# Kernel tuning notes

Measured on AMD Instinct MI355X. Metric: run time of the kernel, lower is better.

## Reference

```python
import jax, jax.numpy as jnp
import numpy as np

B, T, D, H = 8, 1024, 512, 8
QD, PD, POSD, VD, K = 32, 4, 48, 64, 31
FF = 4 * D
FF1, FF2, FF3, NLA = FF * 3 // 4, FF, FF * 5 // 4, D * 3 // 4


def _swoosh_l(x):
    return jax.nn.softplus(x - 4.0) - 0.08 * x - 0.035


def _swoosh_r(x):
    return jax.nn.softplus(x - 1.0) - 0.08 * x - 0.313261687


def setup_inputs() -> dict:
    key = jax.random.key(0)
    ks = iter(jax.random.split(key, 64))

    def w(shape, fan_in):
        return jax.random.normal(next(ks), shape, jnp.float32) * (fan_in ** -0.5)

    inp = {
        'x': jax.random.normal(next(ks), (B, T, D), jnp.float32),
        'pos_emb': jax.random.normal(next(ks), (2 * T - 1, POSD), jnp.float32),
        'mask': jnp.ones((B, T), bool),
        'attw_q_w': w((D, H * QD), D), 'attw_k_w': w((D, H * QD), D),
        'attw_pq_w': w((D, H * PD), D), 'attw_pos_w': w((POSD, H * PD), POSD),
        'ff1_in_w': w((D, FF1), D), 'ff1_in_b': jnp.zeros(FF1),
        'ff1_out_w': w((FF1, D), FF1), 'ff1_out_b': jnp.zeros(D),
        'nla_w': w((D, NLA * 3), D), 'nla_b': jnp.zeros(NLA * 3),
        'nla_out_w': w((NLA, D), NLA), 'nla_out_b': jnp.zeros(D),
        'sa1_v_w': w((D, H * VD), D), 'sa1_v_b': jnp.zeros(H * VD),
        'sa1_o_w': w((H * VD, D), H * VD), 'sa1_o_b': jnp.zeros(D),
        'conv1_in_w': w((D, 2 * D), D), 'conv1_in_b': jnp.zeros(2 * D),
        'conv1_dw_w': w((D, 1, K), K), 'conv1_dw_b': jnp.zeros(D),
        'conv1_out_w': w((D, D), D), 'conv1_out_b': jnp.zeros(D),
        'ff2_in_w': w((D, FF2), D), 'ff2_in_b': jnp.zeros(FF2),
        'ff2_out_w': w((FF2, D), FF2), 'ff2_out_b': jnp.zeros(D),
        'mid_scale': jax.random.uniform(next(ks), (D,), jnp.float32),
        'sa2_v_w': w((D, H * VD), D), 'sa2_v_b': jnp.zeros(H * VD),
        'sa2_o_w': w((H * VD, D), H * VD), 'sa2_o_b': jnp.zeros(D),
        'conv2_in_w': w((D, 2 * D), D), 'conv2_in_b': jnp.zeros(2 * D),
        'conv2_dw_w': w((D, 1, K), K), 'conv2_dw_b': jnp.zeros(D),
        'conv2_out_w': w((D, D), D), 'conv2_out_b': jnp.zeros(D),
        'ff3_in_w': w((D, FF3), D), 'ff3_in_b': jnp.zeros(FF3),
        'ff3_out_w': w((FF3, D), FF3), 'ff3_out_b': jnp.zeros(D),
        'norm_bias': jnp.zeros(D), 'norm_log_scale': jnp.zeros(()),
        'out_scale': jax.random.uniform(next(ks), (D,), jnp.float32),
    }
    return inp


def _forward(x, pos_emb, attw_q_w, attw_k_w, attw_pq_w, attw_pos_w,
             ff1_in_w, ff1_in_b, ff1_out_w, ff1_out_b,
             nla_w, nla_b, nla_out_w, nla_out_b,
             sa1_v_w, sa1_v_b, sa1_o_w, sa1_o_b,
             conv1_in_w, conv1_in_b, conv1_dw_w, conv1_dw_b, conv1_out_w, conv1_out_b,
             ff2_in_w, ff2_in_b, ff2_out_w, ff2_out_b,
             mid_scale,
             sa2_v_w, sa2_v_b, sa2_o_w, sa2_o_b,
             conv2_in_w, conv2_in_b, conv2_dw_w, conv2_dw_b, conv2_out_w, conv2_out_b,
             ff3_in_w, ff3_in_b, ff3_out_w, ff3_out_b,
             norm_bias, norm_log_scale, out_scale, mask):
    res = x
    # --- relative-pos multi-head attention weights ---
    q = (x @ attw_q_w).reshape(B, T, H, QD).transpose(0, 2, 1, 3)
    k = (x @ attw_k_w).reshape(B, T, H, QD).transpose(0, 2, 1, 3)
    p = (x @ attw_pq_w).reshape(B, T, H, PD).transpose(0, 2, 1, 3)
    content = jnp.einsum('bhtd,bhsd->bhts', q, k) * (QD ** -0.5)
    rel = (pos_emb @ attw_pos_w).reshape(2 * T - 1, H, PD).transpose(1, 0, 2)
    idx = jnp.arange(T)[:, None] - jnp.arange(T)[None, :] + (T - 1)
    relg = rel[:, idx]  # [H, T, T, PD]
    scores = content + jnp.einsum('bhtd,htsd->bhts', p, relg)
    scores = jnp.where(mask[:, None, None, :], scores, -10000.0)
    attn = jax.nn.softmax(scores, axis=-1)
    attn = jnp.where(mask[:, None, :, None], attn, 0.0)

    def mk(y):
        return jnp.where(mask[..., None], y, 0.0)

    def ff(y, wi, bi, wo, bo):
        return _swoosh_l(y @ wi + bi) @ wo + bo

    def sa(y, vw, vb, ow, ob):
        v = (y @ vw + vb).reshape(B, T, H, VD).transpose(0, 2, 1, 3)
        o = jnp.einsum('bhts,bhsd->bhtd', attn, v).transpose(0, 2, 1, 3).reshape(B, T, H * VD)
        return o @ ow + ob

    def conv(y, iw, ib, dw, db, ow, ob):
        u = y @ iw + ib
        a, g = jnp.split(u, 2, axis=-1)
        a = (a * jax.nn.sigmoid(g)).transpose(0, 2, 1)  # [B, D, T]
        a = jnp.where(mask[:, None, :], a, 0.0)
        c = jax.lax.conv_general_dilated(a, dw, (1,), [(K // 2, K // 2)],
                                         dimension_numbers=('NCH', 'OIH', 'NCH'),
                                         feature_group_count=D) + db[None, :, None]
        c = _swoosh_r(c.transpose(0, 2, 1))
        return mk(c @ ow + ob)

    def bypass(r, u, s):
        s = jnp.clip(s, 0.2, 1.0)  # eval/steady regime
        return r + (u - r) * s

    x = mk(x + ff(x, ff1_in_w, ff1_in_b, ff1_out_w, ff1_out_b))
    # non-linear attention (uses head 0)
    a, b, c = jnp.split(x @ nla_w + nla_b, 3, axis=-1)
    att0 = jnp.einsum('bts,bsd->btd', attn[:, 0], jnp.tanh(b) * c)
    x = mk(x + ((a * att0) @ nla_out_w + nla_out_b))
    x = mk(x + sa(x, sa1_v_w, sa1_v_b, sa1_o_w, sa1_o_b))
    x = mk(x + conv(x, conv1_in_w, conv1_in_b, conv1_dw_w, conv1_dw_b, conv1_out_w, conv1_out_b))
    x = mk(x + ff(x, ff2_in_w, ff2_in_b, ff2_out_w, ff2_out_b))
    x = mk(bypass(res, x, mid_scale))
    x = mk(x + sa(x, sa2_v_w, sa2_v_b, sa2_o_w, sa2_o_b))
    x = mk(x + conv(x, conv2_in_w, conv2_in_b, conv2_dw_w, conv2_dw_b, conv2_out_w, conv2_out_b))
    x = mk(x + ff(x, ff3_in_w, ff3_in_b, ff3_out_w, ff3_out_b))
    # BiasNorm
    rms = jnp.sqrt(jnp.mean((x - norm_bias) ** 2, axis=-1, keepdims=True) + 1e-8)
    x = x / rms * jnp.exp(norm_log_scale)
    x = mk(bypass(res, x, out_scale))
    return x


def reference(x, pos_emb, mask, attw_q_w, attw_k_w, attw_pq_w, attw_pos_w,
              ff1_in_w, ff1_in_b, ff1_out_w, ff1_out_b,
              nla_w, nla_b, nla_out_w, nla_out_b,
              sa1_v_w, sa1_v_b, sa1_o_w, sa1_o_b,
              conv1_in_w, conv1_in_b, conv1_dw_w, conv1_dw_b, conv1_out_w, conv1_out_b,
              ff2_in_w, ff2_in_b, ff2_out_w, ff2_out_b,
              mid_scale,
              sa2_v_w, sa2_v_b, sa2_o_w, sa2_o_b,
              conv2_in_w, conv2_in_b, conv2_dw_w, conv2_dw_b, conv2_out_w, conv2_out_b,
              ff3_in_w, ff3_in_b, ff3_out_w, ff3_out_b,
              norm_bias, norm_log_scale, out_scale):
    return _forward(x, pos_emb, attw_q_w, attw_k_w, attw_pq_w, attw_pos_w,
                    ff1_in_w, ff1_in_b, ff1_out_w, ff1_out_b,
                    nla_w, nla_b, nla_out_w, nla_out_b,
                    sa1_v_w, sa1_v_b, sa1_o_w, sa1_o_b,
                    conv1_in_w, conv1_in_b, conv1_dw_w, conv1_dw_b, conv1_out_w, conv1_out_b,
                    ff2_in_w, ff2_in_b, ff2_out_w, ff2_out_b,
                    mid_scale,
                    sa2_v_w, sa2_v_b, sa2_o_w, sa2_o_b,
                    conv2_in_w, conv2_in_b, conv2_dw_w, conv2_dw_b, conv2_out_w, conv2_out_b,
                    ff3_in_w, ff3_in_b, ff3_out_w, ff3_out_b,
                    norm_bias, norm_log_scale, out_scale, mask)
```

## Files before the change

### kernel.cpp

```cpp
#include <hip/hip_runtime.h>
#include <hip/hip_bf16.h>
#include <math.h>

using bf16 = __hip_bfloat16;
using f16 = _Float16;
typedef short s16x8 __attribute__((ext_vector_type(8)));
typedef f16   f16x2 __attribute__((ext_vector_type(2)));
typedef float f32x4 __attribute__((ext_vector_type(4)));
typedef unsigned int u32;
#define DEV __device__ __forceinline__
#define AS1 __attribute__((address_space(1)))
#define AS3 __attribute__((address_space(3)))

constexpr int Bc = 8, Tc = 1024, Dc = 512, Hc = 8;
constexpr int QDc = 32, PDc = 4, POSDc = 48, VDc = 64;
constexpr int Nrow = Bc * Tc;
constexpr int KWc = 31;
constexpr float LOG2E = 1.4426950408889634f;

DEV float frcp(float x) { return __builtin_amdgcn_rcpf(x); }
DEV float softplus_f(float y) { return fmaxf(y, 0.f) + __logf(1.f + __expf(-fabsf(y))); }
DEV float swoosh_l_f(float x) { return softplus_f(x - 4.f) - 0.08f * x - 0.035f; }
DEV float swoosh_r_f(float x) { return softplus_f(x - 1.f) - 0.08f * x - 0.313261687f; }
DEV float sigmoid_f(float x)  { return frcp(1.f + __expf(-x)); }
DEV float tanh_f(float x) {
  float e = __expf(2.f * fminf(fmaxf(x, -15.f), 15.f));
  return (e - 1.f) * frcp(e + 1.f);
}
DEV float clip_s(float s)     { return fminf(fmaxf(s, 0.2f), 1.0f); }
DEV float to_f(bf16 x)  { return __bfloat162float(x); }
DEV float b2f(short s) { union { u32 u; float f; } z; z.u = (u32)(unsigned short)s << 16; return z.f; }
DEV short f2bb(float v) { bf16 h = __float2bfloat16(v); return *(short*)&h; }
DEV unsigned short f2h(float v) { f16 h = (f16)v; union { f16 x; unsigned short s; } z; z.x = h; return z.s; }
DEV float h2f(unsigned short s) { union { unsigned short s; f16 x; } z; z.s = s; return (float)z.x; }
DEV u32 packbf(float a, float b) {
  return ((u32)(unsigned short)f2bb(b) << 16) | (u32)(unsigned short)f2bb(a);
}
DEV float dot2(u32 a, u32 b, float c) {
#if __has_builtin(__builtin_amdgcn_fdot2)
  union { u32 u; f16x2 v; } x, y; x.u = a; y.u = b;
  return __builtin_amdgcn_fdot2(x.v, y.v, c, false);
#else
  return c + h2f(a & 0xffff) * h2f(b & 0xffff) + h2f(a >> 16) * h2f(b >> 16);
#endif
}

DEV float wave_sum(float v) {
#pragma unroll
  for (int o = 32; o > 0; o >>= 1) v += __shfl_xor(v, o);
  return v;
}

DEV void gload16(const void* g, void* l) {
  __builtin_amdgcn_global_load_lds((const AS1 u32*)g, (AS3 u32*)l, 16, 0, 0);
}

template <int ACT, int WM, int WN, int FM, int FN>
__global__ __launch_bounds__(256) void gemm_mfma(
    const bf16* __restrict__ A, const bf16* __restrict__ B,
    const float* __restrict__ bias, const float* __restrict__ resid,
    float* __restrict__ Cf, bf16* __restrict__ Cb, bf16* __restrict__ Cb2,
    const bf16* __restrict__ auxb, const float* __restrict__ auxf,
    const float* __restrict__ auxf2,
    int M, int N, int K, int lda, int ldb, int ldc,
    long sAz, long sBo, long sBi, long sCo, long sCi, int nh) {
  constexpr int BM = WM * FM * 16, BN = WN * FN * 16;
  constexpr int NPA = (ACT == 8) ? 3 : 1;
  constexpr int NPB = (ACT == 2) ? 2 : 1;
  constexpr int PANA = 384, PANB = 512;
  constexpr int ASZT = NPA * BM * 128;
  constexpr int BUF = (NPA * BM + NPB * BN) * 128;
  constexpr int LPS = NPA * (BM / 32) + NPB * (BN / 32);

  int z = blockIdx.z;
  int zo = z / nh, zi = z - zo * nh;
  A += (long)z * sAz;
  B += (long)zo * sBo + (long)zi * sBi;
  long coff = (long)zo * sCo + (long)zi * sCi;

  __shared__ char lds[2 * BUF];

  int tid = threadIdx.x;
  int lane = tid & 63, w = tid >> 6;
  int wm = w / WN, wn = w % WN;

  int gx = gridDim.x;
  int nwg = gx * gridDim.y;
  int flat = blockIdx.y * gx + blockIdx.x;
  if ((nwg & 7) == 0) flat = (flat & 7) * (nwg >> 3) + (flat >> 3);
  int m0 = (flat / gx) * BM, n0 = (flat % gx) * BN;

  int lrow = lane >> 3, lch = lane & 7;
  const bf16* ga = A + (long)(m0 + w * (BM / 4) + lrow) * lda + ((lch ^ lrow) << 3);
  const bf16* gb = B + (long)(n0 + w * (BN / 4) + lrow) * ldb + ((lch ^ lrow) << 3);

  f32x4 acc[NPA * NPB][FM][FN];
#pragma unroll
  for (int p = 0; p < NPA * NPB; ++p)
#pragma unroll
    for (int i = 0; i < FM; ++i)
#pragma unroll
      for (int j = 0; j < FN; ++j) acc[p][i][j] = 0.f;

  int nt = K >> 6;
  {
#pragma unroll
    for (int pa = 0; pa < NPA; ++pa) {
      const bf16* gp = ga + (long)(pa * PANA) * lda;
      char* la = lds + pa * BM * 128 + w * (BM / 4) * 128;
#pragma unroll
      for (int i = 0; i < BM / 32; ++i) gload16(gp + (long)(i * 8) * lda, la + i * 1024);
    }
#pragma unroll
    for (int pb = 0; pb < NPB; ++pb) {
      const bf16* gp = gb + (long)(pb * PANB) * ldb;
      char* lb = lds + ASZT + pb * BN * 128 + w * (BN / 4) * 128;
#pragma unroll
      for (int i = 0; i < BN / 32; ++i) gload16(gp + (long)(i * 8) * ldb, lb + i * 1024);
    }
  }

  for (int t = 0; t < nt; ++t) {
    char* cA = lds + (t & 1) * BUF;
    if (t + 1 < nt) {
      int k0 = (t + 1) << 6;
      char* base = lds + ((t + 1) & 1) * BUF;
#pragma unroll
      for (int pa = 0; pa < NPA; ++pa) {
        const bf16* gp = ga + (long)(pa * PANA) * lda + k0;
        char* la = base + pa * BM * 128 + w * (BM / 4) * 128;
#pragma unroll
        for (int i = 0; i < BM / 32; ++i) gload16(gp + (long)(i * 8) * lda, la + i * 1024);
      }
#pragma unroll
      for (int pb = 0; pb < NPB; ++pb) {
        const bf16* gp = gb + (long)(pb * PANB) * ldb + k0;
        char* lb = base + ASZT + pb * BN * 128 + w * (BN / 4) * 128;
#pragma unroll
        for (int i = 0; i < BN / 32; ++i) gload16(gp + (long)(i * 8) * ldb, lb + i * 1024);
      }
      asm volatile("s_waitcnt vmcnt(%0)" :: "n"(LPS) : "memory");
    } else {
      asm volatile("s_waitcnt vmcnt(0)" ::: "memory");
    }
    __builtin_amdgcn_s_barrier();
    __builtin_amdgcn_sched_barrier(0);
#pragma unroll
    for (int ks = 0; ks < 2; ++ks) {
      int cg = ks * 4 + (lane >> 4);
      s16x8 af[NPA][FM], bfr[NPB][FN];
#pragma unroll
      for (int pa = 0; pa < NPA; ++pa)
#pragma unroll
        for (int f = 0; f < FM; ++f) {
          int row = wm * FM * 16 + f * 16 + (lane & 15);
          af[pa][f] = *(const s16x8*)(cA + pa * BM * 128 + row * 128 +
                                      ((cg ^ (row & 7)) << 4));
        }
#pragma unroll
      for (int pb = 0; pb < NPB; ++pb)
#pragma unroll
        for (int f = 0; f < FN; ++f) {
          int row = wn * FN * 16 + f * 16 + (lane & 15);
          bfr[pb][f] = *(const s16x8*)(cA + ASZT + pb * BN * 128 + row * 128 +
                                       ((cg ^ (row & 7)) << 4));
        }
#pragma unroll
      for (int pa = 0; pa < NPA; ++pa)
#pragma unroll
        for (int pb = 0; pb < NPB; ++pb)
#pragma unroll
          for (int fm = 0; fm < FM; ++fm)
#pragma unroll
            for (int fn = 0; fn < FN; ++fn)
              acc[pa * NPB + pb][fm][fn] = __builtin_amdgcn_mfma_f32_16x16x32_bf16(
                  af[pa][fm], bfr[pb][fn], acc[pa * NPB + pb][fm][fn], 0, 0, 0);
    }
    __builtin_amdgcn_sched_barrier(0);
    __builtin_amdgcn_s_barrier();
  }

  int rbase = m0 + wm * FM * 16 + (lane >> 4) * 4;
  int cbase = n0 + wn * FN * 16 + (lane & 15);
#pragma unroll
  for (int fn = 0; fn < FN; ++fn) {
    int col = cbase + fn * 16;
    if (col >= N) continue;
#pragma unroll
    for (int fm = 0; fm < FM; ++fm) {
#pragma unroll
      for (int r = 0; r < 4; ++r) {
        int row = rbase + fm * 16 + r;
        if (row >= M) continue;
        long ci = coff + (long)row * ldc + col;
        if constexpr (ACT == 2) {
          float va = acc[0][fm][fn][r] + bias[col];
          float vg = acc[1][fm][fn][r] + bias[col + 512];
          Cb[ci] = __float2bfloat16(va * sigmoid_f(vg));
        } else if constexpr (ACT == 4) {
          float a = to_f(auxb[(long)col * 8192 + (long)zo * 1024 + row]);
          Cb[ci] = __float2bfloat16(acc[0][fm][fn][r] * a);
        } else if constexpr (ACT == 5) {
          float v = acc[0][fm][fn][r] + bias[col] + resid[ci];
          float rv = auxf[ci];
          float o = rv + (v - rv) * clip_s(auxf2[col]);
          Cf[ci] = o;
          Cb[ci] = __float2bfloat16(o);
        } else if constexpr (ACT == 7) {
          Cb[ci] = __float2bfloat16(acc[0][fm][fn][r] + bias[row]);
        } else if constexpr (ACT == 8) {
          float va = acc[0][fm][fn][r] + bias[row];
          float vb = acc[1][fm][fn][r] + bias[row + 384];
          float vc = acc[2][fm][fn][r] + bias[row + 768];
          Cb2[ci] = __float2bfloat16(va);
          Cb[ci] = __float2bfloat16(tanh_f(vb) * vc);
        } else if constexpr (ACT == 9) {
          float v = acc[0][fm][fn][r];
          if (col < 512) {
            Cb2[(long)row * 512 + col] = __float2bfloat16(v);
          } else {
            Cb[(long)row * ldc + (col - 512)] =
                __float2bfloat16(swoosh_l_f(v + bias[col - 512]));
          }
        } else {
          float v = acc[0][fm][fn][r] + (bias ? bias[col] : 0.f);
          if (ACT == 1) v = swoosh_l_f(v);
          if (resid) v += resid[ci];
          if (Cf) Cf[ci] = v;
          if (Cb) Cb[ci] = __float2bfloat16(v);
        }
      }
    }
  }
}

__global__ __launch_bounds__(256) void relph_kernel(
    const float* __restrict__ pos_emb, const float* __restrict__ Wpos,
    float* __restrict__ relb,
    const float* __restrict__ x0, const float* __restrict__ Wpq,
    f16* __restrict__ ph) {
  int zz = blockIdx.z;
  const float* A  = zz ? x0 : pos_emb;
  const float* Bm = zz ? Wpq : Wpos;
  int M = zz ? Nrow : (2 * Tc - 1);
  int K = zz ? Dc : POSDc;
  int lda = K;
  int m0 = blockIdx.y * 64;
  if (m0 >= M) return;

  __shared__ float As[16][72];
  __shared__ float Bs[16][72];
  int tid = threadIdx.x;
  int tx = tid & 15, ty = tid >> 4;
  int arow = tid >> 2, ak4 = (tid & 3) * 4;
  int bk = tid >> 4, bn4 = (tid & 15) * 4;
  float acc[4][4] = {};
  for (int k0 = 0; k0 < K; k0 += 16) {
    int gm = m0 + arow;
#pragma unroll
    for (int j = 0; j < 4; ++j) {
      int gk = k0 + ak4 + j;
      As[ak4 + j][arow] = (gm < M && gk < K) ? A[(long)gm * lda + gk] : 0.f;
    }
    int gk = k0 + bk;
#pragma unroll
    for (int j = 0; j < 4; ++j) {
      int gn = bn4 + j;
      Bs[bk][bn4 + j] = (gk < K && gn < 32) ? Bm[(long)gk * 32 + gn] : 0.f;
    }
    __syncthreads();
#pragma unroll
    for (int kk = 0; kk < 16; ++kk) {
      float a4[4], b4[4];
#pragma unroll
      for (int i = 0; i < 4; ++i) a4[i] = As[kk][ty * 4 + i];
#pragma unroll
      for (int i = 0; i < 4; ++i) b4[i] = Bs[kk][tx * 4 + i];
#pragma unroll
      for (int i = 0; i < 4; ++i)
#pragma unroll
        for (int j = 0; j < 4; ++j) acc[i][j] += a4[i] * b4[j];
    }
    __syncthreads();
  }
#pragma unroll
  for (int i = 0; i < 4; ++i) {
    int gm = m0 + ty * 4 + i;
    if (gm >= M) continue;
#pragma unroll
    for (int j = 0; j < 4; ++j) {
      int gn = tx * 4 + j;
      if (gn < 32) {
        if (zz) ph[(long)gm * 32 + gn] = (f16)(acc[i][j] * LOG2E);
        else    relb[(long)gm * 32 + gn] = acc[i][j];
      }
    }
  }
}

struct TDesc { const float* src; bf16* dst; int K, N, tile0, ntx; float scale; };
struct TBatch { TDesc d[18]; int n; };

__global__ __launch_bounds__(256) void transpose_batch_kernel(TBatch tb) {
  int tile = blockIdx.x;
  int wi = 0;
#pragma unroll 1
  for (int i = 1; i < 18; ++i)
    if (i < tb.n && tb.d[i].tile0 <= tile) wi = i;
  const float* W = tb.d[wi].src;
  bf16* WT = tb.d[wi].dst;
  int K = tb.d[wi].K, N = tb.d[wi].N;
  float sc = tb.d[wi].scale;
  int lt = tile - tb.d[wi].tile0;
  int ntx = tb.d[wi].ntx;
  int bx = (lt % ntx) * 32, by = (lt / ntx) * 32;

  __shared__ float t[32][33];
  int lx = threadIdx.x & 31, ly = threadIdx.x >> 5;
#pragma unroll
  for (int j = 0; j < 4; ++j) {
    int k = by + ly + j * 8, n = bx + lx;
    if (k < K && n < N) t[ly + j * 8][lx] = W[(long)k * N + n];
  }
  __syncthreads();
#pragma unroll
  for (int j = 0; j < 4; ++j) {
    int n = bx + ly + j * 8, k = by + lx;
    if (n < N && k < K) WT[(long)n * K + k] = __float2bfloat16(t[lx][ly + j * 8] * sc);
  }
}

__global__ void dw_transpose_kernel(const float* __restrict__ dw1, float* __restrict__ o1,
                                    const float* __restrict__ dw2, float* __restrict__ o2) {
  int i = blockIdx.x * 256 + threadIdx.x;
  if (i >= 2 * 512 * KWc) return;
  const float* s = (i < 512 * KWc) ? dw1 : dw2;
  float* o = (i < 512 * KWc) ? o1 : o2;
  int j = (i < 512 * KWc) ? i : i - 512 * KWc;
  int d = j / KWc, kk = j - d * KWc;
  o[kk * 512 + d] = s[j];
}

__global__ void f2b_kernel(const float* __restrict__ in, bf16* __restrict__ out, int nOct) {
  int i = blockIdx.x * 256 + threadIdx.x;
  if (i >= nOct) return;
  float4 a = *(const float4*)(in + (long)i * 8);
  float4 b = *(const float4*)(in + (long)i * 8 + 4);
  s16x8 o;
  o[0] = f2bb(a.x); o[1] = f2bb(a.y); o[2] = f2bb(a.z); o[3] = f2bb(a.w);
  o[4] = f2bb(b.x); o[5] = f2bb(b.y); o[6] = f2bb(b.z); o[7] = f2bb(b.w);
  *(s16x8*)((short*)out + (long)i * 8) = o;
}

__global__ __launch_bounds__(256) void scores_softmax_fused(
    const bf16* __restrict__ qk, const f16* __restrict__ ph,
    const float* __restrict__ rel, bf16* __restrict__ attn) {
  int bh = blockIdx.y;
  int h = bh & (Hc - 1), b = bh >> 3;
  int t0 = blockIdx.x * 16;
  int tid = threadIdx.x, lane = tid & 63, w = tid >> 6;

  __shared__ unsigned short eS[16 * 1024];
  __shared__ u32 rel01[1040], rel23[1040];
  __shared__ u32 pS[16][2];
  __shared__ float lS[16][4];

  for (int i = tid; i < 1039; i += 256) {
    float4 rv = *(const float4*)(rel + (long)(t0 + i) * 32 + h * 4);
    rel01[i] = ((u32)f2h(rv.y) << 16) | f2h(rv.x);
    rel23[i] = ((u32)f2h(rv.w) << 16) | f2h(rv.z);
  }
  if (tid < 16) {
    const u32* pp = (const u32*)(ph + ((long)(b * Tc + t0 + tid)) * 32 + h * 4);
    pS[tid][0] = pp[0]; pS[tid][1] = pp[1];
  }
  __syncthreads();

  s16x8 af = *(const s16x8*)(qk + ((long)(b * Tc + t0 + (lane & 15))) * 512 +
                             h * QDc + (lane >> 4) * 8);
  int g = lane >> 4;
  u32 p01[4], p23[4];
#pragma unroll
  for (int r = 0; r < 4; ++r) { p01[r] = pS[g * 4 + r][0]; p23[r] = pS[g * 4 + r][1]; }
  float sum[4] = {0.f, 0.f, 0.f, 0.f};
  f32x4 zero = {0.f, 0.f, 0.f, 0.f};
  int cols0 = w * 256;
#pragma unroll 4
  for (int tile = 0; tile < 16; ++tile) {
    int s0 = cols0 + tile * 16;
    s16x8 bfr = *(const s16x8*)(qk + ((long)(b * Tc + s0 + (lane & 15))) * 512 +
                                256 + h * QDc + (lane >> 4) * 8);
    f32x4 acc = __builtin_amdgcn_mfma_f32_16x16x32_bf16(af, bfr, zero, 0, 0, 0);
    int scol = s0 + (lane & 15);
    int idx0 = g * 4 - scol + 1023;
#pragma unroll
    for (int r = 0; r < 4; ++r) {
      int idx = idx0 + r;
      float pos = dot2(p23[r], rel23[idx], dot2(p01[r], rel01[idx], 0.f));
      float e = exp2f(acc[r] + pos);
      sum[r] += e;
      *(unsigned short*)((char*)eS + (g * 4 + r) * 2048 + ((scol * 2) ^ (g << 5))) =
          (unsigned short)f2bb(e);
    }
  }
#pragma unroll
  for (int o = 1; o < 16; o <<= 1)
#pragma unroll
    for (int r = 0; r < 4; ++r) sum[r] += __shfl_xor(sum[r], o);
  if ((lane & 15) == 0) {
#pragma unroll
    for (int r = 0; r < 4; ++r) lS[g * 4 + r][w] = sum[r];
  }
  __syncthreads();

#pragma unroll
  for (int rr = 0; rr < 4; ++rr) {
    int row = w * 4 + rr;
    float inv = frcp(lS[row][0] + lS[row][1] + lS[row][2] + lS[row][3]);
    int mask = ((row >> 2) & 3) << 5;
    char* rowbase = (char*)eS + row * 2048;
    u32* grow = (u32*)(attn + ((long)bh * Tc + t0 + row) * Tc);
#pragma unroll
    for (int k = 0; k < 8; ++k) {
      u32 ew = *(u32*)(rowbase + (((lane + k * 64) * 4) ^ mask));
      grow[lane + k * 64] = packbf(b2f((short)(ew & 0xffff)) * inv,
                                   b2f((short)(ew >> 16)) * inv);
    }
  }
}

__global__ __launch_bounds__(256) void dwconv_kernel(
    const bf16* __restrict__ a, const float* __restrict__ dwT,
    const float* __restrict__ db, bf16* __restrict__ c) {
  int i = blockIdx.x * 256 + threadIdx.x;
  int oct = i & 63, bt = i >> 6;
  int t = bt & (Tc - 1), b0 = bt - t;
  float acc0 = db[oct * 8 + 0], acc1 = db[oct * 8 + 1], acc2 = db[oct * 8 + 2],
        acc3 = db[oct * 8 + 3], acc4 = db[oct * 8 + 4], acc5 = db[oct * 8 + 5],
        acc6 = db[oct * 8 + 6], acc7 = db[oct * 8 + 7];
#pragma unroll
  for (int kk = 0; kk < KWc; ++kk) {
    int tt = t + kk - (KWc / 2);
    if ((unsigned)tt < (unsigned)Tc) {
      s16x8 av = *(const s16x8*)((const short*)a + ((long)(b0 + tt) << 9) + oct * 8);
      const float* wp = dwT + kk * 512 + oct * 8;
      float4 w0 = *(const float4*)wp, w1 = *(const float4*)(wp + 4);
      acc0 += b2f(av[0]) * w0.x; acc1 += b2f(av[1]) * w0.y;
      acc2 += b2f(av[2]) * w0.z; acc3 += b2f(av[3]) * w0.w;
      acc4 += b2f(av[4]) * w1.x; acc5 += b2f(av[5]) * w1.y;
      acc6 += b2f(av[6]) * w1.z; acc7 += b2f(av[7]) * w1.w;
    }
  }
  s16x8 o;
  o[0] = f2bb(swoosh_r_f(acc0)); o[1] = f2bb(swoosh_r_f(acc1));
  o[2] = f2bb(swoosh_r_f(acc2)); o[3] = f2bb(swoosh_r_f(acc3));
  o[4] = f2bb(swoosh_r_f(acc4)); o[5] = f2bb(swoosh_r_f(acc5));
  o[6] = f2bb(swoosh_r_f(acc6)); o[7] = f2bb(swoosh_r_f(acc7));
  *(s16x8*)((short*)c + (long)bt * 512 + oct * 8) = o;
}

__global__ __launch_bounds__(256) void rmsnorm_bypass_kernel(
    const float* __restrict__ x, const float* __restrict__ x0,
    const float* __restrict__ nb, const float* __restrict__ nls,
    const float* __restrict__ os, float* __restrict__ out) {
  int row = blockIdx.x;
  int tid = threadIdx.x;
  const float* xr = x + (long)row * 512;
  const float* rr = x0 + (long)row * 512;
  float* orow = out + (long)row * 512;
  float v0 = xr[tid], v1 = xr[tid + 256];
  float d0 = v0 - nb[tid], d1 = v1 - nb[tid + 256];
  float ss = d0 * d0 + d1 * d1;
  __shared__ float red[4];
  int lane = tid & 63, wid = tid >> 6;
  ss = wave_sum(ss);
  if (lane == 0) red[wid] = ss;
  __syncthreads();
  ss = red[0] + red[1] + red[2] + red[3];
  float rms = sqrtf(ss * (1.f / 512.f) + 1e-8f);
  float scl = expf(nls[0]) / rms;
  float r0 = rr[tid], s0 = clip_s(os[tid]);
  orow[tid] = r0 + (v0 * scl - r0) * s0;
  float r1 = rr[tid + 256], s1 = clip_s(os[tid + 256]);
  orow[tid + 256] = r1 + (v1 * scl - r1) * s1;
}

static inline int cdiv(int a, int b) { return (a + b - 1) / b; }

template <int ACT, int WM = 2, int WN = 2, int FM = 2, int FN = 2>
static void mfma_launch(hipStream_t st, const bf16* A, const bf16* B, const float* bias,
                        const float* resid, float* Cf, bf16* Cb, bf16* Cb2,
                        const bf16* auxb, const float* auxf, const float* auxf2,
                        int M, int N, int K, int lda, int ldb, int ldc,
                        int Z = 1, int nh = 1, long sAz = 0, long sBo = 0, long sBi = 0,
                        long sCo = 0, long sCi = 0) {
  dim3 grid(cdiv(N, WN * FN * 16), cdiv(M, WM * FM * 16), Z);
  gemm_mfma<ACT, WM, WN, FM, FN><<<grid, dim3(256), 0, st>>>(
      A, B, bias, resid, Cf, Cb, Cb2, auxb, auxf, auxf2, M, N, K, lda, ldb, ldc,
      sAz, sBo, sBi, sCo, sCi, nh);
}
#define MFMA_AV 2, 2, 2, 2

extern "C" void kernel_launch(void* const* d_in, const int* in_sizes, int n_in,
                              void* d_out, int out_size, void* d_ws, size_t ws_size,
                              hipStream_t stream) {
  const float* x0        = (const float*)d_in[0];
  const float* pos_emb   = (const float*)d_in[1];
  const float* Wq        = (const float*)d_in[3];
  const float* Wk        = (const float*)d_in[4];
  const float* Wpq       = (const float*)d_in[5];
  const float* Wpos      = (const float*)d_in[6];
  const float* ff1_in_w  = (const float*)d_in[7];
  const float* ff1_in_b  = (const float*)d_in[8];
  const float* ff1_out_w = (const float*)d_in[9];
  const float* ff1_out_b = (const float*)d_in[10];
  const float* nla_w     = (const float*)d_in[11];
  const float* nla_b     = (const float*)d_in[12];
  const float* nla_out_w = (const float*)d_in[13];
  const float* nla_out_b = (const float*)d_in[14];
  const float* sa1_v_w   = (const float*)d_in[15];
  const float* sa1_v_b   = (const float*)d_in[16];
  const float* sa1_o_w   = (const float*)d_in[17];
  const float* sa1_o_b   = (const float*)d_in[18];
  const float* cv1_in_w  = (const float*)d_in[19];
  const float* cv1_in_b  = (const float*)d_in[20];
  const float* cv1_dw_w  = (const float*)d_in[21];
  const float* cv1_dw_b  = (const float*)d_in[22];
  const float* cv1_out_w = (const float*)d_in[23];
  const float* cv1_out_b = (const float*)d_in[24];
  const float* ff2_in_w  = (const float*)d_in[25];
  const float* ff2_in_b  = (const float*)d_in[26];
  const float* ff2_out_w = (const float*)d_in[27];
  const float* ff2_out_b = (const float*)d_in[28];
  const float* mid_scale = (const float*)d_in[29];
  const float* sa2_v_w   = (const float*)d_in[30];
  const float* sa2_v_b   = (const float*)d_in[31];
  const float* sa2_o_w   = (const float*)d_in[32];
  const float* sa2_o_b   = (const float*)d_in[33];
  const float* cv2_in_w  = (const float*)d_in[34];
  const float* cv2_in_b  = (const float*)d_in[35];
  const float* cv2_dw_w  = (const float*)d_in[36];
  const float* cv2_dw_b  = (const float*)d_in[37];
  const float* cv2_out_w = (const float*)d_in[38];
  const float* cv2_out_b = (const float*)d_in[39];
  const float* ff3_in_w  = (const float*)d_in[40];
  const float* ff3_in_b  = (const float*)d_in[41];
  const float* ff3_out_w = (const float*)d_in[42];
  const float* ff3_out_b = (const float*)d_in[43];
  const float* norm_bias = (const float*)d_in[44];
  const float* nls       = (const float*)d_in[45];
  const float* out_scale = (const float*)d_in[46];
  float* out = (float*)d_out;

  char* wsb = (char*)d_ws;
  size_t off = 0;
  bf16* attn  = (bf16*)(wsb + off); off += (size_t)Bc * Hc * Tc * Tc * 2;
  float* xA   = (float*)(wsb + off); off += (size_t)Nrow * Dc * 4;
  float* xB   = (float*)(wsb + off); off += (size_t)Nrow * Dc * 4;
  bf16*  xb   = (bf16*)(wsb + off);  off += (size_t)Nrow * Dc * 2;
  bf16*  x0b  = (bf16*)(wsb + off);  off += (size_t)Nrow * Dc * 2;
  bf16*  big1b = (bf16*)(wsb + off); off += (size_t)Nrow * 2560 * 2;
  bf16*  big2b = (bf16*)(wsb + off); off += (size_t)Nrow * Dc * 2;
  bf16*  wT    = (bf16*)(wsb + off); off += (size_t)9961472 * 2;
  float* dwT1  = (float*)(wsb + off); off += (size_t)KWc * 512 * 4;
  float* dwT2  = (float*)(wsb + off); off += (size_t)KWc * 512 * 4;
  bf16*  tbcT  = (bf16*)(wsb + off); off += (size_t)384 * Nrow * 2;
  bf16* big3b = big1b + (size_t)Nrow * 2048;
  bf16* vT    = big2b;
  bf16* qkb   = big2b;
  bf16* aT    = big1b;
  f16*  ph    = (f16*)(big1b + (size_t)Nrow * 1536);
  float* relb = (float*)(ph + (size_t)Nrow * 32);

  bf16* p_w = wT;
  auto alloc_w = [&](int n, int k) { bf16* r = p_w; p_w += (size_t)n * k; return r; };
  bf16* qkff1_wT   = alloc_w(2048, 512);
  bf16* ff1_out_wT = alloc_w(512, 1536);
  bf16* nla_wT     = alloc_w(1152, 512);
  bf16* nla_out_wT = alloc_w(512, 384);
  bf16* sa1_v_wT   = alloc_w(512, 512);
  bf16* sa1_o_wT   = alloc_w(512, 512);
  bf16* cv1_in_wT  = alloc_w(1024, 512);
  bf16* cv1_out_wT = alloc_w(512, 512);
  bf16* ff2_in_wT  = alloc_w(2048, 512);
  bf16* ff2_out_wT = alloc_w(512, 2048);
  bf16* sa2_v_wT   = alloc_w(512, 512);
  bf16* sa2_o_wT   = alloc_w(512, 512);
  bf16* cv2_in_wT  = alloc_w(1024, 512);
  bf16* cv2_out_wT = alloc_w(512, 512);
  bf16* ff3_in_wT  = alloc_w(2560, 512);
  bf16* ff3_out_wT = alloc_w(512, 2560);

  const int nOctD = Nrow * 64;

  f2b_kernel<<<cdiv(nOctD, 256), 256, 0, stream>>>(x0, x0b, nOctD);
  {
    TBatch tb{};
    auto add = [&](int idx, const float* s, bf16* d, int K, int N, int& t0, float sc) {
      tb.d[idx] = {s, d, K, N, t0, cdiv(N, 32), sc};
      t0 += cdiv(N, 32) * cdiv(K, 32);
    };
    int t0 = 0;
    add(0,  Wq,        qkff1_wT,   512, 256,  t0, 0.17677669529663687f * LOG2E);
    add(1,  Wk,        qkff1_wT + (size_t)256 * 512, 512, 256, t0, 1.f);
    add(2,  ff1_in_w,  qkff1_wT + (size_t)512 * 512, 512, 1536, t0, 1.f);
    add(3,  ff1_out_w, ff1_out_wT, 1536, 512, t0, 1.f);
    add(4,  nla_w,     nla_wT,     512, 1152, t0, 1.f);
    add(5,  nla_out_w, nla_out_wT, 384, 512,  t0, 1.f);
    add(6,  sa1_v_w,   sa1_v_wT,   512, 512,  t0, 1.f);
    add(7,  sa1_o_w,   sa1_o_wT,   512, 512,  t0, 1.f);
    add(8,  cv1_in_w,  cv1_in_wT,  512, 1024, t0, 1.f);
    add(9,  cv1_out_w, cv1_out_wT, 512, 512,  t0, 1.f);
    add(10, ff2_in_w,  ff2_in_wT,  512, 2048, t0, 1.f);
    add(11, ff2_out_w, ff2_out_wT, 2048, 512, t0, 1.f);
    add(12, sa2_v_w,   sa2_v_wT,   512, 512,  t0, 1.f);
    add(13, sa2_o_w,   sa2_o_wT,   512, 512,  t0, 1.f);
    add(14, cv2_in_w,  cv2_in_wT,  512, 1024, t0, 1.f);
    add(15, cv2_out_w, cv2_out_wT, 512, 512,  t0, 1.f);
    add(16, ff3_in_w,  ff3_in_wT,  512, 2560, t0, 1.f);
    add(17, ff3_out_w, ff3_out_wT, 2560, 512, t0, 1.f);
    tb.n = 18;
    transpose_batch_kernel<<<t0, 256, 0, stream>>>(tb);
  }
  dw_transpose_kernel<<<cdiv(2 * 512 * KWc, 256), 256, 0, stream>>>(
      cv1_dw_w, dwT1, cv2_dw_w, dwT2);
  relph_kernel<<<dim3(1, 128, 2), 256, 0, stream>>>(pos_emb, Wpos, relb, x0, Wpq, ph);

  mfma_launch<9>(stream, x0b, qkff1_wT, ff1_in_b, nullptr, nullptr, big1b, qkb,
                 nullptr, nullptr, nullptr, Nrow, 2048, 512, 512, 512, 1536);
  scores_softmax_fused<<<dim3(Tc / 16, 64), 256, 0, stream>>>(qkb, ph, relb, attn);

  mfma_launch<0>(stream, big1b, ff1_out_wT, ff1_out_b, x0, xA, xb, nullptr,
                 nullptr, nullptr, nullptr, Nrow, 512, 1536, 1536, 1536, 512);

  mfma_launch<8>(stream, nla_wT, xb, nla_b, nullptr, nullptr, tbcT, aT,
                 nullptr, nullptr, nullptr, 384, Nrow, 512, 512, 512, Nrow);
  mfma_launch<4>(stream, attn, tbcT, nullptr, nullptr, nullptr, big3b, nullptr,
                 aT, nullptr, nullptr, Tc, 384, Tc, Tc, Nrow, 384,
                 Bc, 1, (long)Hc * Tc * Tc, 1024, 0, (long)Tc * 384, 0);
  mfma_launch<0>(stream, big3b, nla_out_wT, nla_out_b, xA, xB, xb, nullptr,
                 nullptr, nullptr, nullptr, Nrow, 512, 384, 384, 384, 512);

  mfma_launch<7>(stream, sa1_v_wT, xb, sa1_v_b, nullptr, nullptr, vT, nullptr,
                 nullptr, nullptr, nullptr, 512, Nrow, 512, 512, 512, Nrow);
  mfma_launch<0, MFMA_AV>(stream, attn, vT, nullptr, nullptr, nullptr, big3b, nullptr,
                          nullptr, nullptr, nullptr, Tc, VDc, Tc, Tc, Nrow, 512,
                          Bc * Hc, Hc, (long)Tc * Tc, Tc, (long)VDc * Nrow,
                          (long)Tc * 512, VDc);
  mfma_launch<0>(stream, big3b, sa1_o_wT, sa1_o_b, xB, xA, xb, nullptr,
                 nullptr, nullptr, nullptr, Nrow, 512, 512, 512, 512, 512);

  mfma_launch<2>(stream, xb, cv1_in_wT, cv1_in_b, nullptr, nullptr, big2b, nullptr,
                 nullptr, nullptr, nullptr, Nrow, 512, 512, 512, 512, 512);
  dwconv_kernel<<<cdiv(nOctD, 256), 256, 0, stream>>>(big2b, dwT1, cv1_dw_b, big3b);
  mfma_launch<0>(stream, big3b, cv1_out_wT, cv1_out_b, xA, xB, xb, nullptr,
                 nullptr, nullptr, nullptr, Nrow, 512, 512, 512, 512, 512);

  mfma_launch<1>(stream, xb, ff2_in_wT, ff2_in_b, nullptr, nullptr, big1b, nullptr,
                 nullptr, nullptr, nullptr, Nrow, 2048, 512, 512, 512, 2048);
  mfma_launch<5>(stream, big1b, ff2_out_wT, ff2_out_b, xB, xB, xb, nullptr,
                 nullptr, x0, mid_scale, Nrow, 512, 2048, 2048, 2048, 512);

  mfma_launch<7>(stream, sa2_v_wT, xb, sa2_v_b, nullptr, nullptr, vT, nullptr,
                 nullptr, nullptr, nullptr, 512, Nrow, 512, 512, 512, Nrow);
  mfma_launch<0, MFMA_AV>(stream, attn, vT, nullptr, nullptr, nullptr, big3b, nullptr,
                          nullptr, nullptr, nullptr, Tc, VDc, Tc, Tc, Nrow, 512,
                          Bc * Hc, Hc, (long)Tc * Tc, Tc, (long)VDc * Nrow,
                          (long)Tc * 512, VDc);
  mfma_launch<0>(stream, big3b, sa2_o_wT, sa2_o_b, xB, xA, xb, nullptr,
                 nullptr, nullptr, nullptr, Nrow, 512, 512, 512, 512, 512);

  mfma_launch<2>(stream, xb, cv2_in_wT, cv2_in_b, nullptr, nullptr, big2b, nullptr,
                 nullptr, nullptr, nullptr, Nrow, 512, 512, 512, 512, 512);
  dwconv_kernel<<<cdiv(nOctD, 256), 256, 0, stream>>>(big2b, dwT2, cv2_dw_b, big3b);
  mfma_launch<0>(stream, big3b, cv2_out_wT, cv2_out_b, xA, xB, xb, nullptr,
                 nullptr, nullptr, nullptr, Nrow, 512, 512, 512, 512, 512);

  mfma_launch<1>(stream, xb, ff3_in_wT, ff3_in_b, nullptr, nullptr, big1b, nullptr,
                 nullptr, nullptr, nullptr, Nrow, 2560, 512, 512, 512, 2560);
  mfma_launch<0>(stream, big1b, ff3_out_wT, ff3_out_b, xB, xA, nullptr, nullptr,
                 nullptr, nullptr, nullptr, Nrow, 512, 2560, 2560, 2560, 512);

  rmsnorm_bypass_kernel<<<Nrow, 256, 0, stream>>>(xA, x0, norm_bias, nls, out_scale, out);
}
```

Before: 765.7 us.

## Defer softmax normalization to consumer GEMM epilogues and precompute fp16 relative-position table

The scores kernel now writes unnormalized exp values and stores per-row inverse sums in a small buffer. The three downstream GEMMs that consume the attention matrix (NLA and both value products) apply the 1/l scale in their epilogues. The relative-position bias is also packed to fp16 pairs per head by relph_kernel, so the scores kernel reads it from global memory instead of staging it through shared memory. This removes per-element multiplies and the LDS staging loop in the softmax kernel, at the cost of extra global loads in the epilogues and uncached per-element relative-position reads.

```diff
diff --git a/kernel.cpp b/kernel.cpp
--- a/kernel.cpp
+++ b/kernel.cpp
@@ -199,7 +199,7 @@
           Cb[ci] = __float2bfloat16(va * sigmoid_f(vg));
         } else if constexpr (ACT == 4) {
           float a = to_f(auxb[(long)col * 8192 + (long)zo * 1024 + row]);
-          Cb[ci] = __float2bfloat16(acc[0][fm][fn][r] * a);
+          Cb[ci] = __float2bfloat16(acc[0][fm][fn][r] * a * auxf[(long)zo * 8192 + row]);
         } else if constexpr (ACT == 5) {
           float v = acc[0][fm][fn][r] + bias[col] + resid[ci];
           float rv = auxf[ci];
@@ -222,6 +222,8 @@
             Cb[(long)row * ldc + (col - 512)] =
                 __float2bfloat16(swoosh_l_f(v + bias[col - 512]));
           }
+        } else if constexpr (ACT == 10) {
+          Cb[ci] = __float2bfloat16(acc[0][fm][fn][r] * auxf[(long)z * 1024 + row]);
         } else {
           float v = acc[0][fm][fn][r] + (bias ? bias[col] : 0.f);
           if (ACT == 1) v = swoosh_l_f(v);
@@ -236,7 +238,7 @@
 
 __global__ __launch_bounds__(256) void relph_kernel(
     const float* __restrict__ pos_emb, const float* __restrict__ Wpos,
-    float* __restrict__ relb,
+    uint2* __restrict__ relh,
     const float* __restrict__ x0, const float* __restrict__ Wpq,
     f16* __restrict__ ph) {
   int zz = blockIdx.z;
@@ -283,17 +285,26 @@
     }
     __syncthreads();
   }
-#pragma unroll
-  for (int i = 0; i < 4; ++i) {
-    int gm = m0 + ty * 4 + i;
-    if (gm >= M) continue;
-#pragma unroll
-    for (int j = 0; j < 4; ++j) {
-      int gn = tx * 4 + j;
-      if (gn < 32) {
-        if (zz) ph[(long)gm * 32 + gn] = (f16)(acc[i][j] * LOG2E);
-        else    relb[(long)gm * 32 + gn] = acc[i][j];
+  if (zz) {
+#pragma unroll
+    for (int i = 0; i < 4; ++i) {
+      int gm = m0 + ty * 4 + i;
+      if (gm >= M) continue;
+#pragma unroll
+      for (int j = 0; j < 4; ++j) {
+        int gn = tx * 4 + j;
+        if (gn < 32) ph[(long)gm * 32 + gn] = (f16)(acc[i][j] * LOG2E);
       }
+    }
+  } else if (tx < 8) {
+#pragma unroll
+    for (int i = 0; i < 4; ++i) {
+      int gm = m0 + ty * 4 + i;
+      if (gm >= M) continue;
+      uint2 rv;
+      rv.x = ((u32)f2h(acc[i][1]) << 16) | f2h(acc[i][0]);
+      rv.y = ((u32)f2h(acc[i][3]) << 16) | f2h(acc[i][2]);
+      relh[(long)tx * 2048 + gm] = rv;
     }
   }
 }
@@ -354,22 +365,17 @@
 
 __global__ __launch_bounds__(256) void scores_softmax_fused(
     const bf16* __restrict__ qk, const f16* __restrict__ ph,
-    const float* __restrict__ rel, bf16* __restrict__ attn) {
+    const uint2* __restrict__ relh, bf16* __restrict__ attn,
+    float* __restrict__ invl) {
   int bh = blockIdx.y;
   int h = bh & (Hc - 1), b = bh >> 3;
   int t0 = blockIdx.x * 16;
   int tid = threadIdx.x, lane = tid & 63, w = tid >> 6;
 
   __shared__ unsigned short eS[16 * 1024];
-  __shared__ u32 rel01[1040], rel23[1040];
   __shared__ u32 pS[16][2];
   __shared__ float lS[16][4];
 
-  for (int i = tid; i < 1039; i += 256) {
-    float4 rv = *(const float4*)(rel + (long)(t0 + i) * 32 + h * 4);
-    rel01[i] = ((u32)f2h(rv.y) << 16) | f2h(rv.x);
-    rel23[i] = ((u32)f2h(rv.w) << 16) | f2h(rv.z);
-  }
   if (tid < 16) {
     const u32* pp = (const u32*)(ph + ((long)(b * Tc + t0 + tid)) * 32 + h * 4);
     pS[tid][0] = pp[0]; pS[tid][1] = pp[1];
@@ -384,6 +390,7 @@
   for (int r = 0; r < 4; ++r) { p01[r] = pS[g * 4 + r][0]; p23[r] = pS[g * 4 + r][1]; }
   float sum[4] = {0.f, 0.f, 0.f, 0.f};
   f32x4 zero = {0.f, 0.f, 0.f, 0.f};
+  const uint2* relb = relh + (long)h * 2048;
   int cols0 = w * 256;
 #pragma unroll 4
   for (int tile = 0; tile < 16; ++tile) {
@@ -392,11 +399,11 @@
                                 256 + h * QDc + (lane >> 4) * 8);
     f32x4 acc = __builtin_amdgcn_mfma_f32_16x16x32_bf16(af, bfr, zero, 0, 0, 0);
     int scol = s0 + (lane & 15);
-    int idx0 = g * 4 - scol + 1023;
+    int idx0 = t0 + g * 4 - scol + 1023;
 #pragma unroll
     for (int r = 0; r < 4; ++r) {
-      int idx = idx0 + r;
-      float pos = dot2(p23[r], rel23[idx], dot2(p01[r], rel01[idx], 0.f));
+      uint2 rr = relb[idx0 + r];
+      float pos = dot2(p23[r], rr.y, dot2(p01[r], rr.x, 0.f));
       float e = exp2f(acc[r] + pos);
       sum[r] += e;
       *(unsigned short*)((char*)eS + (g * 4 + r) * 2048 + ((scol * 2) ^ (g << 5))) =
@@ -416,16 +423,15 @@
 #pragma unroll
   for (int rr = 0; rr < 4; ++rr) {
     int row = w * 4 + rr;
-    float inv = frcp(lS[row][0] + lS[row][1] + lS[row][2] + lS[row][3]);
+    if (lane == 0)
+      invl[(long)bh * 1024 + t0 + row] =
+          frcp(lS[row][0] + lS[row][1] + lS[row][2] + lS[row][3]);
     int mask = ((row >> 2) & 3) << 5;
     char* rowbase = (char*)eS + row * 2048;
     u32* grow = (u32*)(attn + ((long)bh * Tc + t0 + row) * Tc);
 #pragma unroll
-    for (int k = 0; k < 8; ++k) {
-      u32 ew = *(u32*)(rowbase + (((lane + k * 64) * 4) ^ mask));
-      grow[lane + k * 64] = packbf(b2f((short)(ew & 0xffff)) * inv,
-                                   b2f((short)(ew >> 16)) * inv);
-    }
+    for (int k = 0; k < 8; ++k)
+      grow[lane + k * 64] = *(u32*)(rowbase + (((lane + k * 64) * 4) ^ mask));
   }
 }
 
@@ -565,12 +571,13 @@
   float* dwT1  = (float*)(wsb + off); off += (size_t)KWc * 512 * 4;
   float* dwT2  = (float*)(wsb + off); off += (size_t)KWc * 512 * 4;
   bf16*  tbcT  = (bf16*)(wsb + off); off += (size_t)384 * Nrow * 2;
+  float* invl  = (float*)(wsb + off); off += (size_t)64 * 1024 * 4;
+  uint2* relh  = (uint2*)(wsb + off); off += (size_t)8 * 2048 * 8;
   bf16* big3b = big1b + (size_t)Nrow * 2048;
   bf16* vT    = big2b;
   bf16* qkb   = big2b;
   bf16* aT    = big1b;
   f16*  ph    = (f16*)(big1b + (size_t)Nrow * 1536);
-  float* relb = (float*)(ph + (size_t)Nrow * 32);
 
   bf16* p_w = wT;
   auto alloc_w = [&](int n, int k) { bf16* r = p_w; p_w += (size_t)n * k; return r; };
@@ -624,11 +631,11 @@
   }
   dw_transpose_kernel<<<cdiv(2 * 512 * KWc, 256), 256, 0, stream>>>(
       cv1_dw_w, dwT1, cv2_dw_w, dwT2);
-  relph_kernel<<<dim3(1, 128, 2), 256, 0, stream>>>(pos_emb, Wpos, relb, x0, Wpq, ph);
+  relph_kernel<<<dim3(1, 128, 2), 256, 0, stream>>>(pos_emb, Wpos, relh, x0, Wpq, ph);
 
   mfma_launch<9>(stream, x0b, qkff1_wT, ff1_in_b, nullptr, nullptr, big1b, qkb,
                  nullptr, nullptr, nullptr, Nrow, 2048, 512, 512, 512, 1536);
-  scores_softmax_fused<<<dim3(Tc / 16, 64), 256, 0, stream>>>(qkb, ph, relb, attn);
+  scores_softmax_fused<<<dim3(Tc / 16, 64), 256, 0, stream>>>(qkb, ph, relh, attn, invl);
 
   mfma_launch<0>(stream, big1b, ff1_out_wT, ff1_out_b, x0, xA, xb, nullptr,
                  nullptr, nullptr, nullptr, Nrow, 512, 1536, 1536, 1536, 512);
@@ -636,17 +643,17 @@
   mfma_launch<8>(stream, nla_wT, xb, nla_b, nullptr, nullptr, tbcT, aT,
                  nullptr, nullptr, nullptr, 384, Nrow, 512, 512, 512, Nrow);
   mfma_launch<4>(stream, attn, tbcT, nullptr, nullptr, nullptr, big3b, nullptr,
-                 aT, nullptr, nullptr, Tc, 384, Tc, Tc, Nrow, 384,
+                 aT, invl, nullptr, Tc, 384, Tc, Tc, Nrow, 384,
                  Bc, 1, (long)Hc * Tc * Tc, 1024, 0, (long)Tc * 384, 0);
   mfma_launch<0>(stream, big3b, nla_out_wT, nla_out_b, xA, xB, xb, nullptr,
                  nullptr, nullptr, nullptr, Nrow, 512, 384, 384, 384, 512);
 
   mfma_launch<7>(stream, sa1_v_wT, xb, sa1_v_b, nullptr, nullptr, vT, nullptr,
                  nullptr, nullptr, nullptr, 512, Nrow, 512, 512, 512, Nrow);
-  mfma_launch<0, MFMA_AV>(stream, attn, vT, nullptr, nullptr, nullptr, big3b, nullptr,
-                          nullptr, nullptr, nullptr, Tc, VDc, Tc, Tc, Nrow, 512,
-                          Bc * Hc, Hc, (long)Tc * Tc, Tc, (long)VDc * Nrow,
-                          (long)Tc * 512, VDc);
+  mfma_launch<10, MFMA_AV>(stream, attn, vT, nullptr, nullptr, nullptr, big3b, nullptr,
+                           nullptr, invl, nullptr, Tc, VDc, Tc, Tc, Nrow, 512,
+                           Bc * Hc, Hc, (long)Tc * Tc, Tc, (long)VDc * Nrow,
+                           (long)Tc * 512, VDc);
   mfma_launch<0>(stream, big3b, sa1_o_wT, sa1_o_b, xB, xA, xb, nullptr,
                  nullptr, nullptr, nullptr, Nrow, 512, 512, 512, 512, 512);
 
@@ -663,10 +670,10 @@
 
   mfma_launch<7>(stream, sa2_v_wT, xb, sa2_v_b, nullptr, nullptr, vT, nullptr,
                  nullptr, nullptr, nullptr, 512, Nrow, 512, 512, 512, Nrow);
-  mfma_launch<0, MFMA_AV>(stream, attn, vT, nullptr, nullptr, nullptr, big3b, nullptr,
-                          nullptr, nullptr, nullptr, Tc, VDc, Tc, Tc, Nrow, 512,
-                          Bc * Hc, Hc, (long)Tc * Tc, Tc, (long)VDc * Nrow,
-                          (long)Tc * 512, VDc);
+  mfma_launch<10, MFMA_AV>(stream, attn, vT, nullptr, nullptr, nullptr, big3b, nullptr,
+                           nullptr, invl, nullptr, Tc, VDc, Tc, Tc, Nrow, 512,
+                           Bc * Hc, Hc, (long)Tc * Tc, Tc, (long)VDc * Nrow,
+                           (long)Tc * 512, VDc);
   mfma_launch<0>(stream, big3b, sa2_o_wT, sa2_o_b, xB, xA, xb, nullptr,
                  nullptr, nullptr, nullptr, Nrow, 512, 512, 512, 512, 512);
 
```

New measurement: 765.4 us. No clear change (-0.0%).
